# Performance work log

Measured on AMD Instinct MI355X. Metric: run time of the kernel, lower is better.

Reference implementation:

```python
import jax, jax.numpy as jnp
import numpy as np

B, T, L = 256, 512, 40
VOCAB, ED, NC, H = 30000, 8, 22, 64
IN = ED + NC + 1  # GRUCell input: embed + cont + vanco feedback


def setup_inputs():
    key = jax.random.key(0)
    ks = jax.random.split(key, 10)
    cont = jax.random.uniform(ks[0], (B, T, NC), dtype=jnp.float32)
    cat = jax.random.randint(ks[1], (B, T, L), 0, VOCAB, dtype=jnp.int32)
    lb = jax.random.uniform(ks[2], (B, T), dtype=jnp.float32)
    mask = jax.random.randint(ks[3], (B, T), 0, 2, dtype=jnp.int32)
    d = jax.random.uniform(ks[4], (B, T), dtype=jnp.float32)
    td = jax.random.uniform(ks[5], (B, T), dtype=jnp.float32)
    emb = jax.random.normal(ks[6], (VOCAB, ED), dtype=jnp.float32) * 0.1
    emb = emb.at[0].set(0.0)  # padding_idx=0
    W_ih = jax.random.normal(ks[7], (3 * H, IN), dtype=jnp.float32) * 0.1
    W_hh = jax.random.normal(ks[8], (3 * H, H), dtype=jnp.float32) * 0.1
    b_ih = jnp.zeros((3 * H,), jnp.float32)
    b_hh = jnp.zeros((3 * H,), jnp.float32)
    W_out = jax.random.normal(ks[9], (4, H), dtype=jnp.float32) * 0.1
    b_out = jnp.zeros((4,), jnp.float32)
    return dict(cont=cont, cat=cat, lb=lb, mask=mask, d=d, td=td, emb=emb,
                W_ih=W_ih, W_hh=W_hh, b_ih=b_ih, b_hh=b_hh, W_out=W_out, b_out=b_out)


def _forward(cont, cat, lb, mask, d, td, emb, W_ih, W_hh, b_ih, b_hh, W_out, b_out):
    # demographic-derived creatinine clearance, exactly as in the torch code
    age = cont[:, :1, 2] * 16.936469 + 58.239251          # [B,1]
    weight = cont[:, :1, 21] * 30.519849 + 87.5752         # [B,1]
    creat = cont[..., 11] * 1.418099 + 1.314668            # [B,T]
    gender = (cat[:, :1, :] == 5).sum(2).astype(jnp.float32) * 0.15 + 0.85  # [B,1]
    ccl = (140.0 - age) * weight * gender / 72.0 / creat   # [B,T]
    # embedding sum over codes + continuous features
    outEmb = jnp.concatenate([emb[cat].sum(2), cont], axis=2)  # [B,T,ED+NC]
    td24 = td * 24.0
    mf = mask.astype(jnp.float32)
    # step i uses mask/lb of step i-1 for the vanco feedback (0 at i=0)
    mask_prev = jnp.concatenate([jnp.zeros_like(mf[:, :1]), mf[:, :-1]], axis=1)
    lb_prev = jnp.concatenate([jnp.zeros_like(lb[:, :1]), lb[:, :-1]], axis=1)
    Bn = cont.shape[0]

    def step(carry, x):
        h, C, D, A = carry
        e, mp, lp, cc, dd, tt = x
        vfb = jax.lax.stop_gradient(A) * (1.0 - mp) + lp * mp
        xi = jnp.concatenate([e, vfb[:, None]], axis=1)     # [B, IN]
        gi = xi @ W_ih.T + b_ih
        gh = h @ W_hh.T + b_hh
        ir, iz, inn = jnp.split(gi, 3, axis=1)
        hr, hz, hn = jnp.split(gh, 3, axis=1)
        r = jax.nn.sigmoid(ir + hr)
        z = jax.nn.sigmoid(iz + hz)
        n = jnp.tanh(inn + r * hn)
        h = (1.0 - z) * n + z * h                            # GRUCell update
        eta = h @ W_out.T + b_out                            # [B,4]
        e1, e2, e3, e4 = eta[:, 0], eta[:, 1], eta[:, 2], eta[:, 3]
        v1 = 33.1 * jnp.exp(e1)
        k1 = 3.96 * cc / 100.0 * jnp.exp(e2)
        rr = 1000.0 / v1
        v2 = 48.3 * jnp.exp(e4)
        R = -6.99 / 48.3 * jnp.exp(e3)
        k2 = R * v2
        delta = jnp.sqrt((k1 - k2 - R * v1) ** 2 + 4.0 * k1 * R * v1) / v1
        s = (-k1 + k2 + R * v1) / v1
        lam1 = (s - delta) / 2.0
        lam2 = (s + delta) / 2.0
        C1 = rr * (k2 / v1) / lam1 / delta
        C2 = -rr * (k2 / v1) / lam2 / delta
        C3 = -(lam1 - R) / (k2 / v1)
        C4 = -(lam2 - R) / (k2 / v1)
        Cn = ((C + C1) * jnp.exp(lam1 * dd) - C1) * jnp.exp(lam1 * (tt - dd))
        Dn = ((D + C2) * jnp.exp(lam2 * dd) - C2) * jnp.exp(lam2 * (tt - dd))
        An = Cn * C3 + Dn * C4
        return (h, Cn, Dn, An), An

    z0 = jnp.zeros((Bn,), jnp.float32)
    carry0 = (jnp.zeros((Bn, H), jnp.float32), z0, z0, z0)
    xs = (outEmb.transpose(1, 0, 2), mask_prev.T, lb_prev.T, ccl.T, d.T, td24.T)
    _, A_seq = jax.lax.scan(step, carry0, xs)
    return A_seq.T  # [B,T] predicted vancomycin concentration


def reference(cont, cat, lb, mask, d, td, emb, W_ih, W_hh, b_ih, b_hh, W_out, b_out):
    return _forward(cont, cat, lb, mask, d, td, emb, W_ih, W_hh, b_ih, b_hh, W_out, b_out)
```

## Files before the change

### kernel.cpp

```cpp
#include <hip/hip_runtime.h>
#include <math.h>

#define BB 256
#define TT 512
#define LL 40
#define ED 8
#define NC 22
#define HH 64


__global__ void xbuild_kernel(const float* __restrict__ cont, const int* __restrict__ cat,
                              const float* __restrict__ emb, float* __restrict__ X) {
    int p = blockIdx.x * 32 + (threadIdx.x >> 3);
    int e = threadIdx.x & 7;
    const int* cp = cat + (size_t)p * LL;
    float acc = 0.f;
    #pragma unroll 8
    for (int l = 0; l < LL; ++l) acc += emb[cp[l] * ED + e];
    float* xp = X + (size_t)p * 32;
    xp[e] = acc;
    #pragma unroll
    for (int c = e; c < NC; c += 8) xp[8 + c] = cont[(size_t)p * NC + c];
    if (e == 0) { xp[30] = 0.f; xp[31] = 0.f; }
}

__device__ __forceinline__ float fast_rcp(float x) { return __builtin_amdgcn_rcpf(x); }
__device__ __forceinline__ float fast_sig(float x) { return fast_rcp(1.0f + __expf(-x)); }
__device__ __forceinline__ float fast_tanh(float x) {
    float E = __expf(2.0f * x);
    return 1.0f - 2.0f * fast_rcp(E + 1.0f);
}

__device__ __forceinline__ float dpp_add_xor1(float x) {
    int v = __builtin_amdgcn_update_dpp(0, __float_as_int(x), 0xB1, 0xF, 0xF, true);
    return x + __int_as_float(v);
}
__device__ __forceinline__ float dpp_reduce16(float x) {
    int v;
    v = __builtin_amdgcn_update_dpp(0, __float_as_int(x), 0xB1, 0xF, 0xF, true);  x += __int_as_float(v);
    v = __builtin_amdgcn_update_dpp(0, __float_as_int(x), 0x4E, 0xF, 0xF, true);  x += __int_as_float(v);
    v = __builtin_amdgcn_update_dpp(0, __float_as_int(x), 0x141, 0xF, 0xF, true); x += __int_as_float(v);
    v = __builtin_amdgcn_update_dpp(0, __float_as_int(x), 0x140, 0xF, 0xF, true); x += __int_as_float(v);
    return x;
}

__global__ __launch_bounds__(192, 1) void scan_kernel(
    const float* __restrict__ X,
    const int* __restrict__ cat,
    const float* __restrict__ lb, const int* __restrict__ mask,
    const float* __restrict__ dvec, const float* __restrict__ td,
    const float* __restrict__ W_ih, const float* __restrict__ W_hh,
    const float* __restrict__ b_ih, const float* __restrict__ b_hh,
    const float* __restrict__ W_out, const float* __restrict__ b_out,
    float* __restrict__ out)
{
    const int b   = blockIdx.x;
    const int tid = threadIdx.x;

    __shared__ __align__(16) float  feat[TT * 32];
    __shared__ __align__(16) float4 sc[TT];
    __shared__ float  ccl[TT];
    __shared__ __align__(16) float  h_lds[HH];
    __shared__ __align__(16) float  out_lds[TT];
    __shared__ float vfb_lds;
    __shared__ float kb_lds;

    const size_t bT = (size_t)b * TT;

    {
        const float4* Xb4 = (const float4*)(X + bT * 32);
        float4* f4 = (float4*)feat;
        #pragma unroll 4
        for (int i = tid; i < TT * 8; i += 192) f4[i] = Xb4[i];
        for (int i = tid; i < TT; i += 192)
            sc[i] = make_float4(dvec[bT + i], td[bT + i] * 24.0f,
                                (float)mask[bT + i], lb[bT + i]);
        if (tid < HH) h_lds[tid] = 0.f;
        if (tid == 0) vfb_lds = 0.f;
    }
    __syncthreads();
    if (tid < HH) {
        int cv = (tid < LL) ? cat[(size_t)b * TT * LL + tid] : 0;
        unsigned long long bal = __ballot(tid < LL && cv == 5);
        float g   = (float)__popcll(bal) * 0.15f + 0.85f;
        float age = feat[10] * 16.936469f + 58.239251f;
        float wgt = feat[29] * 30.519849f + 87.5752f;
        if (tid == 0) kb_lds = (140.0f - age) * wgt * g / 72.0f;
    }
    __syncthreads();
    {
        const float Kb = kb_lds;
        for (int i = tid; i < TT; i += 192)
            ccl[i] = Kb * fast_rcp(fmaf(feat[i * 32 + 19], 1.418099f, 1.314668f));
    }

    const bool isW12 = (tid >= 64);
    const int  L    = tid - 64;
    const int  half = L & 1;
    const int  jj   = L >> 1;
    const int  ei   = tid & 15, ej = tid >> 4;

    float w0q[3][16], whq[3][32];
    float bsr = 0.f, bsz = 0.f, biN = 0.f, bhN = 0.f;
    float w30r = 0.f, w30z = 0.f, w30n = 0.f;
    float wo0 = 0.f, wo1 = 0.f, wo2 = 0.f, wo3 = 0.f;
    if (isW12) {
        #pragma unroll
        for (int q = 0; q < 3; ++q) {
            const int row = jj + 64 * q;
            #pragma unroll
            for (int k = 0; k < 16; ++k) {
                int f = 16 * half + k;
                w0q[q][k] = (f < 30) ? W_ih[row * 31 + f] : 0.f;
            }
            #pragma unroll
            for (int k = 0; k < 32; ++k)
                whq[q][k] = W_hh[row * 64 + 32 * half + k];
        }
        bsr = b_ih[jj]        + b_hh[jj];
        bsz = b_ih[jj + 64]   + b_hh[jj + 64];
        biN = b_ih[jj + 128];
        bhN = b_hh[jj + 128];
        w30r = W_ih[jj * 31 + 30];
        w30z = W_ih[(jj + 64) * 31 + 30];
        w30n = W_ih[(jj + 128) * 31 + 30];
        #pragma unroll
        for (int q = 0; q < 3; ++q) {
            #pragma unroll
            for (int k = 0; k < 16; ++k) asm volatile("" : "+v"(w0q[q][k]));
            #pragma unroll
            for (int k = 0; k < 32; ++k) asm volatile("" : "+v"(whq[q][k]));
        }
    } else {
        wo0 = W_out[ej * 64 + 4 * ei + 0];
        wo1 = W_out[ej * 64 + 4 * ei + 1];
        wo2 = W_out[ej * 64 + 4 * ei + 2];
        wo3 = W_out[ej * 64 + 4 * ei + 3];
    }
    const float bo0 = b_out[0], bo1 = b_out[1], bo2 = b_out[2], bo3 = b_out[3];

    float hreg = 0.f;
    float Cc = 0.f, Dc = 0.f;
    float a10 = 0.f, a11 = 0.f, a12 = 0.f;
    float a20 = 0.f, a21 = 0.f, a22 = 0.f;

    auto do_dots = [&](int t) {
        const float4* fx = (const float4*)(feat + t * 32) + 4 * half;
        const float4 f0 = fx[0], f1 = fx[1], f2 = fx[2], f3 = fx[3];
        const float4* hx = (const float4*)h_lds + 8 * half;
        const float4 h0 = hx[0], h1 = hx[1], h2 = hx[2], h3 = hx[3];
        const float4 h4 = hx[4], h5 = hx[5], h6 = hx[6], h7 = hx[7];
        float p1[3], p2[3];
        #pragma unroll
        for (int q = 0; q < 3; ++q) {
            float r;
            r = f0.x * w0q[q][0];
            r = fmaf(f0.y, w0q[q][1],  r);
            r = fmaf(f0.z, w0q[q][2],  r);
            r = fmaf(f0.w, w0q[q][3],  r);
            r = fmaf(f1.x, w0q[q][4],  r);
            r = fmaf(f1.y, w0q[q][5],  r);
            r = fmaf(f1.z, w0q[q][6],  r);
            r = fmaf(f1.w, w0q[q][7],  r);
            r = fmaf(f2.x, w0q[q][8],  r);
            r = fmaf(f2.y, w0q[q][9],  r);
            r = fmaf(f2.z, w0q[q][10], r);
            r = fmaf(f2.w, w0q[q][11], r);
            r = fmaf(f3.x, w0q[q][12], r);
            r = fmaf(f3.y, w0q[q][13], r);
            r = fmaf(f3.z, w0q[q][14], r);
            r = fmaf(f3.w, w0q[q][15], r);
            p1[q] = r;
            float s;
            s = h0.x * whq[q][0];
            s = fmaf(h0.y, whq[q][1],  s);
            s = fmaf(h0.z, whq[q][2],  s);
            s = fmaf(h0.w, whq[q][3],  s);
            s = fmaf(h1.x, whq[q][4],  s);
            s = fmaf(h1.y, whq[q][5],  s);
            s = fmaf(h1.z, whq[q][6],  s);
            s = fmaf(h1.w, whq[q][7],  s);
            s = fmaf(h2.x, whq[q][8],  s);
            s = fmaf(h2.y, whq[q][9],  s);
            s = fmaf(h2.z, whq[q][10], s);
            s = fmaf(h2.w, whq[q][11], s);
            s = fmaf(h3.x, whq[q][12], s);
            s = fmaf(h3.y, whq[q][13], s);
            s = fmaf(h3.z, whq[q][14], s);
            s = fmaf(h3.w, whq[q][15], s);
            s = fmaf(h4.x, whq[q][16], s);
            s = fmaf(h4.y, whq[q][17], s);
            s = fmaf(h4.z, whq[q][18], s);
            s = fmaf(h4.w, whq[q][19], s);
            s = fmaf(h5.x, whq[q][20], s);
            s = fmaf(h5.y, whq[q][21], s);
            s = fmaf(h5.z, whq[q][22], s);
            s = fmaf(h5.w, whq[q][23], s);
            s = fmaf(h6.x, whq[q][24], s);
            s = fmaf(h6.y, whq[q][25], s);
            s = fmaf(h6.z, whq[q][26], s);
            s = fmaf(h6.w, whq[q][27], s);
            s = fmaf(h7.x, whq[q][28], s);
            s = fmaf(h7.y, whq[q][29], s);
            s = fmaf(h7.z, whq[q][30], s);
            s = fmaf(h7.w, whq[q][31], s);
            p2[q] = s;
        }
        a10 = dpp_add_xor1(p1[0]);
        a11 = dpp_add_xor1(p1[1]);
        a12 = dpp_add_xor1(p1[2]);
        a20 = dpp_add_xor1(p2[0]);
        a21 = dpp_add_xor1(p2[1]);
        a22 = dpp_add_xor1(p2[2]);
    };

    if (isW12) do_dots(0);

    for (int t = 0; t < TT; ++t) {
        if (isW12) {
            const float vfb = vfb_lds;
            float tr  = a10 + a20 + bsr;
            float tz  = a11 + a21 + bsz;
            float tnn = a12 + biN;
            float pre_r = fmaf(vfb, w30r, tr);
            float pre_z = fmaf(vfb, w30z, tz);
            float r = fast_sig(pre_r);
            float z = fast_sig(pre_z);
            float inn = fmaf(vfb, w30n, tnn);
            float hn  = a22 + bhN;
            float n = fast_tanh(fmaf(r, hn, inn));
            hreg = fmaf(z, hreg - n, n);
            if (half == 0) h_lds[jj] = hreg;
        }
        __syncthreads();

        if (isW12) {
            if (t + 1 < TT) do_dots(t + 1);
        } else {
            const float4 sv = sc[t];
            const float  cc = ccl[t];
            const float4 hv = ((const float4*)h_lds)[ei];
            float p = hv.x * wo0;
            p = fmaf(hv.y, wo1, p);
            p = fmaf(hv.z, wo2, p);
            p = fmaf(hv.w, wo3, p);
            p = dpp_reduce16(p);
            const float e0 = __int_as_float(__builtin_amdgcn_readlane(__float_as_int(p), 0));
            const float e1 = __int_as_float(__builtin_amdgcn_readlane(__float_as_int(p), 16));
            const float e2 = __int_as_float(__builtin_amdgcn_readlane(__float_as_int(p), 32));
            const float e3 = __int_as_float(__builtin_amdgcn_readlane(__float_as_int(p), 48));

            float E1 = __expf(e0 + bo0);
            float E2 = __expf(e1 + bo1);
            float E3 = __expf(e2 + bo2);
            float E4 = __expf(e3 + bo3);
            float v1  = 33.1f * E1;
            float rv1 = fast_rcp(v1);
            float k1  = 3.96f * cc * 0.01f * E2;
            float rrr = 1000.0f * rv1;
            float v2  = 48.3f * E4;
            float R   = (-6.99f / 48.3f) * E3;
            float k2  = R * v2;
            float q   = k1 - k2 - R * v1;
            float disc = fmaf(q, q, 4.0f * k1 * R * v1);
            float delta = __builtin_amdgcn_sqrtf(disc) * rv1;
            float sgm  = (k2 - k1 + R * v1) * rv1;
            float lam1 = (sgm - delta) * 0.5f;
            float lam2 = (sgm + delta) * 0.5f;
            float kv  = k2 * rv1;
            float rkv = fast_rcp(kv);
            float C1  = rrr * kv * fast_rcp(lam1 * delta);
            float C2  = -rrr * kv * fast_rcp(lam2 * delta);
            float C3  = -(lam1 - R) * rkv;
            float C4  = -(lam2 - R) * rkv;
            float dd = sv.x, ttv = sv.y;
            float Cn  = fmaf(Cc + C1, __expf(lam1 * dd), -C1) * __expf(lam1 * (ttv - dd));
            float Dn  = fmaf(Dc + C2, __expf(lam2 * dd), -C2) * __expf(lam2 * (ttv - dd));
            float An  = fmaf(Cn, C3, Dn * C4);
            Cc = Cn; Dc = Dn;
            if (tid == 0) {
                out_lds[t] = An;
                vfb_lds = fmaf(An, 1.0f - sv.z, sv.w * sv.z);
            }
        }
        __syncthreads();
    }

    if (tid < TT / 4) ((float4*)(out + bT))[tid] = ((const float4*)out_lds)[tid];
}

extern "C" void kernel_launch(void* const* d_in, const int* in_sizes, int n_in,
                              void* d_out, int out_size, void* d_ws, size_t ws_size,
                              hipStream_t stream) {
    const float* cont  = (const float*)d_in[0];
    const int*   cat   = (const int*)  d_in[1];
    const float* lb    = (const float*)d_in[2];
    const int*   mask  = (const int*)  d_in[3];
    const float* dvec  = (const float*)d_in[4];
    const float* td    = (const float*)d_in[5];
    const float* emb   = (const float*)d_in[6];
    const float* W_ih  = (const float*)d_in[7];
    const float* W_hh  = (const float*)d_in[8];
    const float* b_ih  = (const float*)d_in[9];
    const float* b_hh  = (const float*)d_in[10];
    const float* W_out = (const float*)d_in[11];
    const float* b_out = (const float*)d_in[12];
    float* out = (float*)d_out;

    float* X = (float*)d_ws;

    hipLaunchKernelGGL(xbuild_kernel, dim3((BB * TT) / 32), dim3(256), 0, stream,
                       cont, cat, emb, X);
    hipLaunchKernelGGL(scan_kernel, dim3(BB), dim3(192), 0, stream,
                       X, cat, lb, mask, dvec, td, W_ih, W_hh, b_ih, b_hh, W_out, b_out, out);
}
```

Measured before the change: 397.0 us.

## Fuse feature build into scan kernel and split GRU dots four ways per unit

Removes the separate xbuild kernel and its workspace round-trip by gathering the embeddings and staging the continuous features directly into LDS inside the scan kernel. The GRU dot products are redistributed from 2 to 4 lanes per hidden unit (320 threads), each lane covering 24 input/hidden elements for all three gates, with quad DPP reductions. Weights are prescaled by log2(e) so the gates and PK exponentials use exp2 directly, and the hidden buffer is padded to reduce bank conflicts. The scan critical path gets shorter per step, at the cost of doing the embedding gather inside only 256 blocks.

```diff
diff --git a/kernel.cpp b/kernel.cpp
--- a/kernel.cpp
+++ b/kernel.cpp
@@ -7,34 +7,24 @@
 #define ED 8
 #define NC 22
 #define HH 64
-
-
-__global__ void xbuild_kernel(const float* __restrict__ cont, const int* __restrict__ cat,
-                              const float* __restrict__ emb, float* __restrict__ X) {
-    int p = blockIdx.x * 32 + (threadIdx.x >> 3);
-    int e = threadIdx.x & 7;
-    const int* cp = cat + (size_t)p * LL;
-    float acc = 0.f;
-    #pragma unroll 8
-    for (int l = 0; l < LL; ++l) acc += emb[cp[l] * ED + e];
-    float* xp = X + (size_t)p * 32;
-    xp[e] = acc;
-    #pragma unroll
-    for (int c = e; c < NC; c += 8) xp[8 + c] = cont[(size_t)p * NC + c];
-    if (e == 0) { xp[30] = 0.f; xp[31] = 0.f; }
-}
-
-__device__ __forceinline__ float fast_rcp(float x) { return __builtin_amdgcn_rcpf(x); }
-__device__ __forceinline__ float fast_sig(float x) { return fast_rcp(1.0f + __expf(-x)); }
-__device__ __forceinline__ float fast_tanh(float x) {
-    float E = __expf(2.0f * x);
-    return 1.0f - 2.0f * fast_rcp(E + 1.0f);
-}
+#define BLK 320
+
+#define L2E 1.4426950408889634f
+#define S2E 2.8853900817779268f
+
+__device__ __forceinline__ float fast_rcp(float x)  { return __builtin_amdgcn_rcpf(x); }
+__device__ __forceinline__ float fast_exp2(float x) { return __builtin_amdgcn_exp2f(x); }
 
 __device__ __forceinline__ float dpp_add_xor1(float x) {
     int v = __builtin_amdgcn_update_dpp(0, __float_as_int(x), 0xB1, 0xF, 0xF, true);
     return x + __int_as_float(v);
 }
+__device__ __forceinline__ float dpp_add_xor2(float x) {
+    int v = __builtin_amdgcn_update_dpp(0, __float_as_int(x), 0x4E, 0xF, 0xF, true);
+    return x + __int_as_float(v);
+}
+__device__ __forceinline__ float quad_sum(float x) { return dpp_add_xor2(dpp_add_xor1(x)); }
+
 __device__ __forceinline__ float dpp_reduce16(float x) {
     int v;
     v = __builtin_amdgcn_update_dpp(0, __float_as_int(x), 0xB1, 0xF, 0xF, true);  x += __int_as_float(v);
@@ -44,11 +34,11 @@
     return x;
 }
 
-__global__ __launch_bounds__(192, 1) void scan_kernel(
-    const float* __restrict__ X,
-    const int* __restrict__ cat,
+__global__ __launch_bounds__(BLK, 1) void scan_kernel(
+    const float* __restrict__ cont, const int* __restrict__ cat,
     const float* __restrict__ lb, const int* __restrict__ mask,
     const float* __restrict__ dvec, const float* __restrict__ td,
+    const float* __restrict__ emb,
     const float* __restrict__ W_ih, const float* __restrict__ W_hh,
     const float* __restrict__ b_ih, const float* __restrict__ b_hh,
     const float* __restrict__ W_out, const float* __restrict__ b_out,
@@ -57,189 +47,168 @@
     const int b   = blockIdx.x;
     const int tid = threadIdx.x;
 
-    __shared__ __align__(16) float  feat[TT * 32];
-    __shared__ __align__(16) float4 sc[TT];
-    __shared__ float  ccl[TT];
-    __shared__ __align__(16) float  h_lds[HH];
-    __shared__ __align__(16) float  out_lds[TT];
+    __shared__ __align__(128) float  feat[TT * 32];
+    __shared__ __align__(16)  float4 sc[TT];
+    __shared__ float  cclA[TT];
+    __shared__ __align__(128) float hbuf[72];
+    __shared__ __align__(16) float out_lds[TT];
     __shared__ float vfb_lds;
     __shared__ float kb_lds;
 
-    const size_t bT = (size_t)b * TT;
-
-    {
-        const float4* Xb4 = (const float4*)(X + bT * 32);
-        float4* f4 = (float4*)feat;
-        #pragma unroll 4
-        for (int i = tid; i < TT * 8; i += 192) f4[i] = Xb4[i];
-        for (int i = tid; i < TT; i += 192)
-            sc[i] = make_float4(dvec[bT + i], td[bT + i] * 24.0f,
-                                (float)mask[bT + i], lb[bT + i]);
-        if (tid < HH) h_lds[tid] = 0.f;
-        if (tid == 0) vfb_lds = 0.f;
-    }
-    __syncthreads();
-    if (tid < HH) {
-        int cv = (tid < LL) ? cat[(size_t)b * TT * LL + tid] : 0;
+    const size_t bT    = (size_t)b * TT;
+    const int*   catb  = cat  + bT * LL;
+    const float* contb = cont + bT * NC;
+
+    const bool isDot = (tid >= 64);
+    const int  Ld = tid - 64;
+    const int  j  = Ld >> 2;
+    const int  q  = Ld & 3;
+    const int  ei = tid & 15, ej = tid >> 4;
+
+    float wr_[24], wz_[24], wn_[24];
+    float br = 0.f, bz = 0.f, bnx = 0.f, bnh = 0.f;
+    float w30r = 0.f, w30z = 0.f, w30n = 0.f;
+    float wo0 = 0.f, wo1 = 0.f, wo2 = 0.f, wo3 = 0.f;
+    if (isDot) {
+        #pragma unroll
+        for (int m = 0; m < 24; ++m) {
+            const int f = 24 * q + m;
+            float a, c, d;
+            if (f < 30)      { a = W_ih[j*31+f]; c = W_ih[(j+64)*31+f]; d = W_ih[(j+128)*31+f]; }
+            else if (f < 32) { a = 0.f; c = 0.f; d = 0.f; }
+            else             { a = W_hh[j*64+f-32]; c = W_hh[(j+64)*64+f-32]; d = W_hh[(j+128)*64+f-32]; }
+            wr_[m] = a * L2E;
+            wz_[m] = c * L2E;
+            wn_[m] = d * S2E;
+        }
+        #pragma unroll
+        for (int m = 0; m < 24; ++m) {
+            asm volatile("" : "+v"(wr_[m]));
+            asm volatile("" : "+v"(wz_[m]));
+            asm volatile("" : "+v"(wn_[m]));
+        }
+        br   = (b_ih[j]      + b_hh[j])      * L2E;
+        bz   = (b_ih[j + 64] + b_hh[j + 64]) * L2E;
+        bnx  = b_ih[j + 128] * S2E;
+        bnh  = b_hh[j + 128] * S2E;
+        w30r = W_ih[j*31 + 30]        * L2E;
+        w30z = W_ih[(j+64)*31 + 30]   * L2E;
+        w30n = W_ih[(j+128)*31 + 30]  * S2E;
+    } else {
+        wo0 = W_out[ej * 64 + 4*ei + 0] * L2E;
+        wo1 = W_out[ej * 64 + 4*ei + 1] * L2E;
+        wo2 = W_out[ej * 64 + 4*ei + 2] * L2E;
+        wo3 = W_out[ej * 64 + 4*ei + 3] * L2E;
+    }
+    const float boL0 = b_out[0] * L2E, boL1 = b_out[1] * L2E;
+    const float boL2 = b_out[2] * L2E, boL3 = b_out[3] * L2E;
+
+    for (int i = tid; i < TT * NC; i += BLK) {
+        int r = i / NC, c = i - r * NC;
+        feat[r * 32 + 8 + c] = contb[i];
+    }
+    for (int i = tid; i < TT; i += BLK) {
+        feat[i * 32 + 30] = 0.f;
+        feat[i * 32 + 31] = 0.f;
+    }
+    for (int i = tid; i < TT * 8; i += BLK) {
+        int r = i >> 3, e = i & 7;
+        const int* cp = catb + r * LL;
+        float acc = 0.f;
+        #pragma unroll 8
+        for (int l = 0; l < LL; ++l) acc += emb[cp[l] * ED + e];
+        feat[r * 32 + e] = acc;
+    }
+    for (int i = tid; i < TT; i += BLK) {
+        float d   = dvec[bT + i];
+        float t24 = td[bT + i] * 24.0f;
+        sc[i] = make_float4(d * L2E, (t24 - d) * L2E, (float)mask[bT + i], lb[bT + i]);
+    }
+    if (tid < 72) hbuf[tid] = 0.f;
+    if (tid == 0) vfb_lds = 0.f;
+    if (tid < 64) {
+        int cv = (tid < LL) ? catb[tid] : 0;
         unsigned long long bal = __ballot(tid < LL && cv == 5);
         float g   = (float)__popcll(bal) * 0.15f + 0.85f;
-        float age = feat[10] * 16.936469f + 58.239251f;
-        float wgt = feat[29] * 30.519849f + 87.5752f;
+        float age = contb[2]  * 16.936469f + 58.239251f;
+        float wgt = contb[21] * 30.519849f + 87.5752f;
         if (tid == 0) kb_lds = (140.0f - age) * wgt * g / 72.0f;
     }
     __syncthreads();
     {
         const float Kb = kb_lds;
-        for (int i = tid; i < TT; i += 192)
-            ccl[i] = Kb * fast_rcp(fmaf(feat[i * 32 + 19], 1.418099f, 1.314668f));
-    }
-
-    const bool isW12 = (tid >= 64);
-    const int  L    = tid - 64;
-    const int  half = L & 1;
-    const int  jj   = L >> 1;
-    const int  ei   = tid & 15, ej = tid >> 4;
-
-    float w0q[3][16], whq[3][32];
-    float bsr = 0.f, bsz = 0.f, biN = 0.f, bhN = 0.f;
-    float w30r = 0.f, w30z = 0.f, w30n = 0.f;
-    float wo0 = 0.f, wo1 = 0.f, wo2 = 0.f, wo3 = 0.f;
-    if (isW12) {
-        #pragma unroll
-        for (int q = 0; q < 3; ++q) {
-            const int row = jj + 64 * q;
-            #pragma unroll
-            for (int k = 0; k < 16; ++k) {
-                int f = 16 * half + k;
-                w0q[q][k] = (f < 30) ? W_ih[row * 31 + f] : 0.f;
-            }
-            #pragma unroll
-            for (int k = 0; k < 32; ++k)
-                whq[q][k] = W_hh[row * 64 + 32 * half + k];
-        }
-        bsr = b_ih[jj]        + b_hh[jj];
-        bsz = b_ih[jj + 64]   + b_hh[jj + 64];
-        biN = b_ih[jj + 128];
-        bhN = b_hh[jj + 128];
-        w30r = W_ih[jj * 31 + 30];
-        w30z = W_ih[(jj + 64) * 31 + 30];
-        w30n = W_ih[(jj + 128) * 31 + 30];
-        #pragma unroll
-        for (int q = 0; q < 3; ++q) {
-            #pragma unroll
-            for (int k = 0; k < 16; ++k) asm volatile("" : "+v"(w0q[q][k]));
-            #pragma unroll
-            for (int k = 0; k < 32; ++k) asm volatile("" : "+v"(whq[q][k]));
-        }
-    } else {
-        wo0 = W_out[ej * 64 + 4 * ei + 0];
-        wo1 = W_out[ej * 64 + 4 * ei + 1];
-        wo2 = W_out[ej * 64 + 4 * ei + 2];
-        wo3 = W_out[ej * 64 + 4 * ei + 3];
-    }
-    const float bo0 = b_out[0], bo1 = b_out[1], bo2 = b_out[2], bo3 = b_out[3];
+        for (int i = tid; i < TT; i += BLK)
+            cclA[i] = Kb * fast_rcp(fmaf(contb[i * NC + 11], 1.418099f, 1.314668f));
+    }
+    __syncthreads();
 
     float hreg = 0.f;
     float Cc = 0.f, Dc = 0.f;
-    float a10 = 0.f, a11 = 0.f, a12 = 0.f;
-    float a20 = 0.f, a21 = 0.f, a22 = 0.f;
+    float sr = 0.f, sz = 0.f, snx = 0.f, snh = 0.f;
+    float4 svc = make_float4(0.f, 0.f, 0.f, 0.f);
+    float  ccv = 0.f;
+
+    const float4* hA4 = (const float4*)hbuf;
+    const float4* hB4 = (const float4*)(hbuf + 36);
 
     auto do_dots = [&](int t) {
-        const float4* fx = (const float4*)(feat + t * 32) + 4 * half;
-        const float4 f0 = fx[0], f1 = fx[1], f2 = fx[2], f3 = fx[3];
-        const float4* hx = (const float4*)h_lds + 8 * half;
-        const float4 h0 = hx[0], h1 = hx[1], h2 = hx[2], h3 = hx[3];
-        const float4 h4 = hx[4], h5 = hx[5], h6 = hx[6], h7 = hx[7];
-        float p1[3], p2[3];
+        const float4* f4t = (const float4*)(feat + t * 32);
+        float ra = 0.f, za = 0.f, nxa = 0.f, nha = 0.f;
         #pragma unroll
-        for (int q = 0; q < 3; ++q) {
-            float r;
-            r = f0.x * w0q[q][0];
-            r = fmaf(f0.y, w0q[q][1],  r);
-            r = fmaf(f0.z, w0q[q][2],  r);
-            r = fmaf(f0.w, w0q[q][3],  r);
-            r = fmaf(f1.x, w0q[q][4],  r);
-            r = fmaf(f1.y, w0q[q][5],  r);
-            r = fmaf(f1.z, w0q[q][6],  r);
-            r = fmaf(f1.w, w0q[q][7],  r);
-            r = fmaf(f2.x, w0q[q][8],  r);
-            r = fmaf(f2.y, w0q[q][9],  r);
-            r = fmaf(f2.z, w0q[q][10], r);
-            r = fmaf(f2.w, w0q[q][11], r);
-            r = fmaf(f3.x, w0q[q][12], r);
-            r = fmaf(f3.y, w0q[q][13], r);
-            r = fmaf(f3.z, w0q[q][14], r);
-            r = fmaf(f3.w, w0q[q][15], r);
-            p1[q] = r;
-            float s;
-            s = h0.x * whq[q][0];
-            s = fmaf(h0.y, whq[q][1],  s);
-            s = fmaf(h0.z, whq[q][2],  s);
-            s = fmaf(h0.w, whq[q][3],  s);
-            s = fmaf(h1.x, whq[q][4],  s);
-            s = fmaf(h1.y, whq[q][5],  s);
-            s = fmaf(h1.z, whq[q][6],  s);
-            s = fmaf(h1.w, whq[q][7],  s);
-            s = fmaf(h2.x, whq[q][8],  s);
-            s = fmaf(h2.y, whq[q][9],  s);
-            s = fmaf(h2.z, whq[q][10], s);
-            s = fmaf(h2.w, whq[q][11], s);
-            s = fmaf(h3.x, whq[q][12], s);
-            s = fmaf(h3.y, whq[q][13], s);
-            s = fmaf(h3.z, whq[q][14], s);
-            s = fmaf(h3.w, whq[q][15], s);
-            s = fmaf(h4.x, whq[q][16], s);
-            s = fmaf(h4.y, whq[q][17], s);
-            s = fmaf(h4.z, whq[q][18], s);
-            s = fmaf(h4.w, whq[q][19], s);
-            s = fmaf(h5.x, whq[q][20], s);
-            s = fmaf(h5.y, whq[q][21], s);
-            s = fmaf(h5.z, whq[q][22], s);
-            s = fmaf(h5.w, whq[q][23], s);
-            s = fmaf(h6.x, whq[q][24], s);
-            s = fmaf(h6.y, whq[q][25], s);
-            s = fmaf(h6.z, whq[q][26], s);
-            s = fmaf(h6.w, whq[q][27], s);
-            s = fmaf(h7.x, whq[q][28], s);
-            s = fmaf(h7.y, whq[q][29], s);
-            s = fmaf(h7.z, whq[q][30], s);
-            s = fmaf(h7.w, whq[q][31], s);
-            p2[q] = s;
-        }
-        a10 = dpp_add_xor1(p1[0]);
-        a11 = dpp_add_xor1(p1[1]);
-        a12 = dpp_add_xor1(p1[2]);
-        a20 = dpp_add_xor1(p2[0]);
-        a21 = dpp_add_xor1(p2[1]);
-        a22 = dpp_add_xor1(p2[2]);
+        for (int k = 0; k < 6; ++k) {
+            const int idx = 6 * q + k;
+            const float4* pH = (idx < 16) ? (hA4 + (idx - 8)) : (hB4 + (idx - 16));
+            const float4* p  = (idx < 8) ? (f4t + idx) : pH;
+            const float4 uv = *p;
+            ra = fmaf(uv.x, wr_[4*k+0], ra);
+            ra = fmaf(uv.y, wr_[4*k+1], ra);
+            ra = fmaf(uv.z, wr_[4*k+2], ra);
+            ra = fmaf(uv.w, wr_[4*k+3], ra);
+            za = fmaf(uv.x, wz_[4*k+0], za);
+            za = fmaf(uv.y, wz_[4*k+1], za);
+            za = fmaf(uv.z, wz_[4*k+2], za);
+            za = fmaf(uv.w, wz_[4*k+3], za);
+            if (idx < 8) {
+                nxa = fmaf(uv.x, wn_[4*k+0], nxa);
+                nxa = fmaf(uv.y, wn_[4*k+1], nxa);
+                nxa = fmaf(uv.z, wn_[4*k+2], nxa);
+                nxa = fmaf(uv.w, wn_[4*k+3], nxa);
+            } else {
+                nha = fmaf(uv.x, wn_[4*k+0], nha);
+                nha = fmaf(uv.y, wn_[4*k+1], nha);
+                nha = fmaf(uv.z, wn_[4*k+2], nha);
+                nha = fmaf(uv.w, wn_[4*k+3], nha);
+            }
+        }
+        sr  = quad_sum(ra);
+        sz  = quad_sum(za);
+        snx = quad_sum(nxa);
+        snh = quad_sum(nha);
     };
 
-    if (isW12) do_dots(0);
+    if (isDot) do_dots(0);
 
     for (int t = 0; t < TT; ++t) {
-        if (isW12) {
+        if (isDot) {
             const float vfb = vfb_lds;
-            float tr  = a10 + a20 + bsr;
-            float tz  = a11 + a21 + bsz;
-            float tnn = a12 + biN;
-            float pre_r = fmaf(vfb, w30r, tr);
-            float pre_z = fmaf(vfb, w30z, tz);
-            float r = fast_sig(pre_r);
-            float z = fast_sig(pre_z);
-            float inn = fmaf(vfb, w30n, tnn);
-            float hn  = a22 + bhN;
-            float n = fast_tanh(fmaf(r, hn, inn));
+            float prer = sr + br + vfb * w30r;
+            float prez = sz + bz + vfb * w30z;
+            float r = fast_rcp(1.0f + fast_exp2(-prer));
+            float z = fast_rcp(1.0f + fast_exp2(-prez));
+            float yp = snx + bnx + vfb * w30n + r * (snh + bnh);
+            float n = 1.0f - 2.0f * fast_rcp(fast_exp2(yp) + 1.0f);
             hreg = fmaf(z, hreg - n, n);
-            if (half == 0) h_lds[jj] = hreg;
+            if (q == 0) hbuf[(j < 32) ? j : (36 + j - 32)] = hreg;
+        } else {
+            svc = sc[t];
+            ccv = cclA[t];
         }
         __syncthreads();
 
-        if (isW12) {
+        if (isDot) {
             if (t + 1 < TT) do_dots(t + 1);
         } else {
-            const float4 sv = sc[t];
-            const float  cc = ccl[t];
-            const float4 hv = ((const float4*)h_lds)[ei];
+            const float4 hv = (ei < 8) ? hA4[ei] : hB4[ei - 8];
             float p = hv.x * wo0;
             p = fmaf(hv.y, wo1, p);
             p = fmaf(hv.z, wo2, p);
@@ -250,19 +219,19 @@
             const float e2 = __int_as_float(__builtin_amdgcn_readlane(__float_as_int(p), 32));
             const float e3 = __int_as_float(__builtin_amdgcn_readlane(__float_as_int(p), 48));
 
-            float E1 = __expf(e0 + bo0);
-            float E2 = __expf(e1 + bo1);
-            float E3 = __expf(e2 + bo2);
-            float E4 = __expf(e3 + bo3);
+            float E1 = fast_exp2(e0 + boL0);
+            float E2 = fast_exp2(e1 + boL1);
+            float E3 = fast_exp2(e2 + boL2);
+            float E4 = fast_exp2(e3 + boL3);
             float v1  = 33.1f * E1;
             float rv1 = fast_rcp(v1);
-            float k1  = 3.96f * cc * 0.01f * E2;
+            float k1  = 0.0396f * ccv * E2;
             float rrr = 1000.0f * rv1;
             float v2  = 48.3f * E4;
             float R   = (-6.99f / 48.3f) * E3;
             float k2  = R * v2;
-            float q   = k1 - k2 - R * v1;
-            float disc = fmaf(q, q, 4.0f * k1 * R * v1);
+            float qq  = k1 - k2 - R * v1;
+            float disc = fmaf(qq, qq, 4.0f * k1 * R * v1);
             float delta = __builtin_amdgcn_sqrtf(disc) * rv1;
             float sgm  = (k2 - k1 + R * v1) * rv1;
             float lam1 = (sgm - delta) * 0.5f;
@@ -273,14 +242,13 @@
             float C2  = -rrr * kv * fast_rcp(lam2 * delta);
             float C3  = -(lam1 - R) * rkv;
             float C4  = -(lam2 - R) * rkv;
-            float dd = sv.x, ttv = sv.y;
-            float Cn  = fmaf(Cc + C1, __expf(lam1 * dd), -C1) * __expf(lam1 * (ttv - dd));
-            float Dn  = fmaf(Dc + C2, __expf(lam2 * dd), -C2) * __expf(lam2 * (ttv - dd));
+            float Cn  = fmaf(Cc + C1, fast_exp2(lam1 * svc.x), -C1) * fast_exp2(lam1 * svc.y);
+            float Dn  = fmaf(Dc + C2, fast_exp2(lam2 * svc.x), -C2) * fast_exp2(lam2 * svc.y);
             float An  = fmaf(Cn, C3, Dn * C4);
             Cc = Cn; Dc = Dn;
             if (tid == 0) {
                 out_lds[t] = An;
-                vfb_lds = fmaf(An, 1.0f - sv.z, sv.w * sv.z);
+                vfb_lds = fmaf(An, 1.0f - svc.z, svc.w * svc.z);
             }
         }
         __syncthreads();
@@ -307,10 +275,7 @@
     const float* b_out = (const float*)d_in[12];
     float* out = (float*)d_out;
 
-    float* X = (float*)d_ws;
-
-    hipLaunchKernelGGL(xbuild_kernel, dim3((BB * TT) / 32), dim3(256), 0, stream,
-                       cont, cat, emb, X);
-    hipLaunchKernelGGL(scan_kernel, dim3(BB), dim3(192), 0, stream,
-                       X, cat, lb, mask, dvec, td, W_ih, W_hh, b_ih, b_hh, W_out, b_out, out);
-}
+    hipLaunchKernelGGL(scan_kernel, dim3(BB), dim3(BLK), 0, stream,
+                       cont, cat, lb, mask, dvec, td, emb, W_ih, W_hh, b_ih, b_hh,
+                       W_out, b_out, out);
+}
```

Result: slower. 476.1 us (+19.9%).
